# Kernel tuning notes

Measured on AMD Instinct MI355X. Metric: run time of the kernel, lower is better.

The kernel has to match this reference:

```python
import jax, jax.numpy as jnp
import numpy as np


def setup_inputs() -> dict:
    key = jax.random.key(0)
    ks = jax.random.split(key, 5)
    d_out, d_in = 4096, 4096
    r = min(d_out, d_in)
    B, T = 4, 2048
    x = jax.random.normal(ks[0], (B, T, d_in), dtype=jnp.float32)
    U = jax.random.normal(ks[1], (d_out, r), dtype=jnp.float32)
    S = jax.random.uniform(ks[2], (r,), dtype=jnp.float32)
    Vt = jax.random.normal(ks[3], (r, d_in), dtype=jnp.float32)
    epsilon = jnp.zeros((r,), dtype=jnp.float32)
    bias = jax.random.normal(ks[4], (d_out,), dtype=jnp.float32)
    return {"x": x, "U": U, "S": S, "Vt": Vt, "epsilon": epsilon, "bias": bias}


def reference(x, U, S, Vt, epsilon, bias):
    # w = U @ diag(S + epsilon) @ Vt  (diag folded as column scale of U)
    w = (U * (S + epsilon)[None, :]) @ Vt  # [d_out, d_in]
    # F.linear: y = x @ w.T + bias
    return jnp.einsum('btk,ok->bto', x, w) + bias
```

## Files before the change

kernel.cpp:

```cpp
#include <hip/hip_runtime.h>
#include <hip/hip_bf16.h>
#include <stdint.h>

typedef __attribute__((ext_vector_type(4))) float f32x4;
typedef __attribute__((ext_vector_type(8))) short short8v;

typedef __attribute__((address_space(1))) void gvoid;
typedef __attribute__((address_space(3))) void lvoid;

#define GLD16(gp, lp) __builtin_amdgcn_global_load_lds((const gvoid*)(gp), (lvoid*)(lp), 16, 0, 0)

__device__ __forceinline__ unsigned short f2bf(float f) {
    union { float ff; unsigned uu; } a; a.ff = f;
    unsigned u = a.uu;
    u += 0x7FFFu + ((u >> 16) & 1u);
    return (unsigned short)(u >> 16);
}

__global__ __launch_bounds__(256) void prep_u_kernel(
    const float* __restrict__ U, const float* __restrict__ S,
    const float* __restrict__ eps, unsigned short* __restrict__ Ub) {
    long idx = ((long)blockIdx.x * 256 + threadIdx.x) * 8;
    int r = (int)(idx & 4095);
    f32x4 u0 = *(const f32x4*)(U + idx);
    f32x4 u1 = *(const f32x4*)(U + idx + 4);
    f32x4 s0 = *(const f32x4*)(S + r);
    f32x4 s1 = *(const f32x4*)(S + r + 4);
    f32x4 e0 = *(const f32x4*)(eps + r);
    f32x4 e1 = *(const f32x4*)(eps + r + 4);
    union { uint4 v; unsigned short s[8]; } o;
#pragma unroll
    for (int j = 0; j < 4; ++j) {
        o.s[j]     = f2bf(u0[j] * (s0[j] + e0[j]));
        o.s[j + 4] = f2bf(u1[j] * (s1[j] + e1[j]));
    }
    *(uint4*)(Ub + idx) = o.v;
}

__global__ __launch_bounds__(256) void cvt_bf16_kernel(
    const float* __restrict__ src, unsigned short* __restrict__ dst) {
    long idx = ((long)blockIdx.x * 256 + threadIdx.x) * 8;
    f32x4 v0 = *(const f32x4*)(src + idx);
    f32x4 v1 = *(const f32x4*)(src + idx + 4);
    union { uint4 v; unsigned short s[8]; } o;
#pragma unroll
    for (int j = 0; j < 4; ++j) {
        o.s[j]     = f2bf(v0[j]);
        o.s[j + 4] = f2bf(v1[j]);
    }
    *(uint4*)(dst + idx) = o.v;
}

__global__ __launch_bounds__(256) void transpose_cvt_kernel(
    const float* __restrict__ src, unsigned short* __restrict__ dst) {
    __shared__ float tile[64][65];
    int tx = threadIdx.x & 63;
    int tq = threadIdx.x >> 6;
    int r0 = blockIdx.y << 6;
    int k0 = blockIdx.x << 6;
#pragma unroll
    for (int i = 0; i < 16; ++i) {
        int row = (i << 2) + tq;
        tile[row][tx] = src[(long)(r0 + row) * 4096 + k0 + tx];
    }
    __syncthreads();
#pragma unroll
    for (int i = 0; i < 16; ++i) {
        int krow = (i << 2) + tq;
        dst[(long)(k0 + krow) * 4096 + r0 + tx] = f2bf(tile[tx][krow]);
    }
}

#define MM(a, b, c) __builtin_amdgcn_mfma_f32_16x16x32_bf16(a, b, c, 0, 0, 0)

#define ACH(bf, kh) (As + ((bf) * 2 + (kh)) * 8192)
#define BCH(bf, kh) (Bs + ((bf) * 2 + (kh)) * 8192)

#define STAGE_A(bf, kh, koff) do { \
    const unsigned short* _s = A + gAr + (koff); \
    unsigned short* _d = ACH(bf, kh) + wave * 512; \
    GLD16(_s, _d); GLD16(_s + (long)128 * K, _d + 4096); } while (0)

#define STAGE_B(bf, kh, koff) do { \
    const unsigned short* _s = B + gBr + (koff); \
    unsigned short* _d = BCH(bf, kh) + wave * 512; \
    GLD16(_s, _d); GLD16(_s + (long)128 * K, _d + 4096); } while (0)

#define LOAD_A2(bf, ks) do { \
    const unsigned short* _p = ACH(bf, ks) + aBase; \
    _Pragma("unroll") \
    for (int _m = 0; _m < 4; ++_m) { \
        aR[0][_m] = *(const short8v*)(_p + _m * 512); \
        aR[1][_m] = *(const short8v*)(_p + _m * 512 + 2048); } } while (0)

#define READ_B(bf, ks) do { \
    const unsigned short* _p = BCH(bf, ks) + bBase; \
    _Pragma("unroll") \
    for (int _n = 0; _n < 4; ++_n) bR[_n] = *(const short8v*)(_p + _n * 512); } while (0)

#define PH_SYNC do { \
    __builtin_amdgcn_s_barrier(); \
    asm volatile("s_waitcnt lgkmcnt(0)" ::: "memory"); } while (0)

#define MFMA32 do { \
    __builtin_amdgcn_s_setprio(1); \
    _Pragma("unroll") \
    for (int _h = 0; _h < 2; ++_h) \
    _Pragma("unroll") \
    for (int _m = 0; _m < 4; ++_m) { \
        acc[_h * 4 + _m][0] = MM(aR[_h][_m], bR[0], acc[_h * 4 + _m][0]); \
        acc[_h * 4 + _m][1] = MM(aR[_h][_m], bR[1], acc[_h * 4 + _m][1]); \
        acc[_h * 4 + _m][2] = MM(aR[_h][_m], bR[2], acc[_h * 4 + _m][2]); \
        acc[_h * 4 + _m][3] = MM(aR[_h][_m], bR[3], acc[_h * 4 + _m][3]); \
    } \
    __builtin_amdgcn_s_setprio(0); } while (0)

#define VM4 asm volatile("s_waitcnt vmcnt(4)" ::: "memory")
#define PH_END __builtin_amdgcn_s_barrier()

template<int OUT_BF16, int BIAS>
__global__ __launch_bounds__(512, 2) void gemm256_kernel(
    const unsigned short* __restrict__ A,
    const unsigned short* __restrict__ B,
    void* __restrict__ Cv, const float* __restrict__ bias,
    int M, int N, int K) {
    __shared__ unsigned short As[4 * 8192];
    __shared__ unsigned short Bs[4 * 8192];

    const int tid  = threadIdx.x;
    const int wave = tid >> 6;
    const int lane = tid & 63;
    const int fr   = lane & 15;
    const int fq   = lane >> 4;

    const int nwg = gridDim.x;
    const int bid = blockIdx.x;
    const int cpx = nwg >> 3;
    const int wg  = (bid & 7) * cpx + (bid >> 3);
    const int ntn = N >> 8;
    const long m0 = (long)(wg / ntn) << 8;
    const long n0 = (long)(wg % ntn) << 8;

    const int wwr = wave >> 2;
    const int wwc = wave & 3;

    const int  rS  = tid >> 2;
    const int  sS  = (tid & 3) ^ ((rS >> 1) & 3);
    const long gAr = (m0 + rS) * K + sS * 8;
    const long gBr = (n0 + rS) * K + sS * 8;

    const int swz   = (fq ^ ((fr >> 1) & 3)) * 8;
    const int aBase = (wwr * 128 + fr) * 32 + swz;
    const int bBase = (wwc * 64 + fr) * 32 + swz;

    f32x4  acc[8][4] = {};
    short8v aR[2][4], bR[4];

    STAGE_A(0, 0, 0);  STAGE_B(0, 0, 0);
    STAGE_A(0, 1, 32); STAGE_B(0, 1, 32);
    STAGE_A(1, 0, 64); STAGE_B(1, 0, 64);
    VM4;
    __builtin_amdgcn_s_barrier();

    const int nIter = K >> 7;
    for (int i = 0; i < nIter; ++i) {
        const int kt1off = 128 * i + 96;
        int k3 = 128 * i + 128; if (k3 >= K) k3 -= K;
        int k5 = 128 * i + 160; if (k5 >= K) k5 -= K;
        int k7 = 128 * i + 192; if (k7 >= K) k7 -= K;

        LOAD_A2(0, 0); READ_B(0, 0); STAGE_A(1, 1, kt1off); STAGE_B(1, 1, kt1off);
        PH_SYNC; MFMA32; PH_END;
        LOAD_A2(0, 1); READ_B(0, 1); STAGE_A(0, 0, k3); STAGE_B(0, 0, k3);
        PH_SYNC; MFMA32; VM4; PH_END;
        LOAD_A2(1, 0); READ_B(1, 0); STAGE_A(0, 1, k5); STAGE_B(0, 1, k5);
        PH_SYNC; MFMA32; PH_END;
        LOAD_A2(1, 1); READ_B(1, 1); STAGE_A(1, 0, k7); STAGE_B(1, 0, k7);
        PH_SYNC; MFMA32; VM4; PH_END;
    }

#pragma unroll
    for (int nf = 0; nf < 4; ++nf) {
        const int col = (int)n0 + wwc * 64 + nf * 16 + fr;
        float bv = BIAS ? bias[col] : 0.0f;
#pragma unroll
        for (int mf = 0; mf < 8; ++mf) {
            f32x4 v = acc[mf][nf];
            long rowb = m0 + wwr * 128 + mf * 16 + fq * 4;
#pragma unroll
            for (int j = 0; j < 4; ++j) {
                float val = v[j] + bv;
                long off = (rowb + j) * N + col;
                if (OUT_BF16) ((unsigned short*)Cv)[off] = f2bf(val);
                else          ((float*)Cv)[off] = val;
            }
        }
    }
}

extern "C" void kernel_launch(void* const* d_in, const int* in_sizes, int n_in,
                              void* d_out, int out_size, void* d_ws, size_t ws_size,
                              hipStream_t stream) {
    const float* x    = (const float*)d_in[0];
    const float* U    = (const float*)d_in[1];
    const float* S    = (const float*)d_in[2];
    const float* Vt   = (const float*)d_in[3];
    const float* eps  = (const float*)d_in[4];
    const float* bias = (const float*)d_in[5];
    float* out = (float*)d_out;

    char* ws = (char*)d_ws;
    unsigned short* Ub  = (unsigned short*)(ws);
    unsigned short* VtT = (unsigned short*)(ws + (size_t)(32 << 20));
    unsigned short* Wb  = (unsigned short*)(ws + (size_t)(64 << 20));
    unsigned short* Xb  = (unsigned short*)(ws);

    prep_u_kernel<<<8192, 256, 0, stream>>>(U, S, eps, Ub);
    transpose_cvt_kernel<<<dim3(64, 64), 256, 0, stream>>>(Vt, VtT);
    gemm256_kernel<1, 0><<<256, 512, 0, stream>>>(Ub, VtT, (void*)Wb, nullptr,
                                                  4096, 4096, 4096);
    cvt_bf16_kernel<<<16384, 256, 0, stream>>>(x, Xb);
    gemm256_kernel<0, 1><<<512, 512, 0, stream>>>(Xb, Wb, (void*)out, bias,
                                                  8192, 4096, 4096);
}
```

Measured before the change: 469.2 us.

## Shrink GEMM tile to 256x128 with triple-buffered 32-K pipeline

Changes the GEMM block tile from 256x256 to 256x128. Each wave now covers 64x64 instead of 128x64, and the LDS staging becomes a 3-stage ring of 32-wide K chunks instead of 4 chunks in double pairs. Launch bounds move to 4 blocks per CU and the grid doubles, aiming for higher occupancy and more wave parallelism to hide memory latency. In exchange each block reuses less data per load and does more barrier phases per unit of work. The loop hardcodes K=4096 (42 groups of 96 plus a 2-step tail).

```diff
diff --git a/kernel.cpp b/kernel.cpp
--- a/kernel.cpp
+++ b/kernel.cpp
@@ -73,28 +73,26 @@
 
 #define MM(a, b, c) __builtin_amdgcn_mfma_f32_16x16x32_bf16(a, b, c, 0, 0, 0)
 
-#define ACH(bf, kh) (As + ((bf) * 2 + (kh)) * 8192)
-#define BCH(bf, kh) (Bs + ((bf) * 2 + (kh)) * 8192)
-
-#define STAGE_A(bf, kh, koff) do { \
+#define ACH(b) (As + (b) * 8192)
+#define BCH(b) (Bs + (b) * 4096)
+
+#define STAGE_A(b, koff) do { \
     const unsigned short* _s = A + gAr + (koff); \
-    unsigned short* _d = ACH(bf, kh) + wave * 512; \
+    unsigned short* _d = ACH(b) + wave * 512; \
     GLD16(_s, _d); GLD16(_s + (long)128 * K, _d + 4096); } while (0)
 
-#define STAGE_B(bf, kh, koff) do { \
+#define STAGE_B(b, koff) do { \
     const unsigned short* _s = B + gBr + (koff); \
-    unsigned short* _d = BCH(bf, kh) + wave * 512; \
-    GLD16(_s, _d); GLD16(_s + (long)128 * K, _d + 4096); } while (0)
-
-#define LOAD_A2(bf, ks) do { \
-    const unsigned short* _p = ACH(bf, ks) + aBase; \
+    unsigned short* _d = BCH(b) + wave * 512; \
+    GLD16(_s, _d); } while (0)
+
+#define LOAD_A(b) do { \
+    const unsigned short* _p = ACH(b) + aBase; \
     _Pragma("unroll") \
-    for (int _m = 0; _m < 4; ++_m) { \
-        aR[0][_m] = *(const short8v*)(_p + _m * 512); \
-        aR[1][_m] = *(const short8v*)(_p + _m * 512 + 2048); } } while (0)
-
-#define READ_B(bf, ks) do { \
-    const unsigned short* _p = BCH(bf, ks) + bBase; \
+    for (int _m = 0; _m < 4; ++_m) aR[_m] = *(const short8v*)(_p + _m * 512); } while (0)
+
+#define READ_B(b) do { \
+    const unsigned short* _p = BCH(b) + bBase; \
     _Pragma("unroll") \
     for (int _n = 0; _n < 4; ++_n) bR[_n] = *(const short8v*)(_p + _n * 512); } while (0)
 
@@ -102,30 +100,33 @@
     __builtin_amdgcn_s_barrier(); \
     asm volatile("s_waitcnt lgkmcnt(0)" ::: "memory"); } while (0)
 
-#define MFMA32 do { \
+#define MFMA16 do { \
     __builtin_amdgcn_s_setprio(1); \
     _Pragma("unroll") \
-    for (int _h = 0; _h < 2; ++_h) \
-    _Pragma("unroll") \
     for (int _m = 0; _m < 4; ++_m) { \
-        acc[_h * 4 + _m][0] = MM(aR[_h][_m], bR[0], acc[_h * 4 + _m][0]); \
-        acc[_h * 4 + _m][1] = MM(aR[_h][_m], bR[1], acc[_h * 4 + _m][1]); \
-        acc[_h * 4 + _m][2] = MM(aR[_h][_m], bR[2], acc[_h * 4 + _m][2]); \
-        acc[_h * 4 + _m][3] = MM(aR[_h][_m], bR[3], acc[_h * 4 + _m][3]); \
+        acc[_m][0] = MM(aR[_m], bR[0], acc[_m][0]); \
+        acc[_m][1] = MM(aR[_m], bR[1], acc[_m][1]); \
+        acc[_m][2] = MM(aR[_m], bR[2], acc[_m][2]); \
+        acc[_m][3] = MM(aR[_m], bR[3], acc[_m][3]); \
     } \
     __builtin_amdgcn_s_setprio(0); } while (0)
 
-#define VM4 asm volatile("s_waitcnt vmcnt(4)" ::: "memory")
+#define VM3 asm volatile("s_waitcnt vmcnt(3)" ::: "memory")
 #define PH_END __builtin_amdgcn_s_barrier()
 
+#define ITER(rb, sb, sk) do { \
+    LOAD_A(rb); READ_B(rb); \
+    STAGE_A(sb, sk); STAGE_B(sb, sk); \
+    PH_SYNC; MFMA16; VM3; PH_END; } while (0)
+
 template<int OUT_BF16, int BIAS>
-__global__ __launch_bounds__(512, 2) void gemm256_kernel(
+__global__ __launch_bounds__(512, 4) void gemm256_kernel(
     const unsigned short* __restrict__ A,
     const unsigned short* __restrict__ B,
     void* __restrict__ Cv, const float* __restrict__ bias,
     int M, int N, int K) {
-    __shared__ unsigned short As[4 * 8192];
-    __shared__ unsigned short Bs[4 * 8192];
+    __shared__ unsigned short As[3 * 8192];
+    __shared__ unsigned short Bs[3 * 4096];
 
     const int tid  = threadIdx.x;
     const int wave = tid >> 6;
@@ -137,12 +138,12 @@
     const int bid = blockIdx.x;
     const int cpx = nwg >> 3;
     const int wg  = (bid & 7) * cpx + (bid >> 3);
-    const int ntn = N >> 8;
+    const int ntn = N >> 7;
     const long m0 = (long)(wg / ntn) << 8;
-    const long n0 = (long)(wg % ntn) << 8;
-
-    const int wwr = wave >> 2;
-    const int wwc = wave & 3;
+    const long n0 = (long)(wg % ntn) << 7;
+
+    const int wwr = wave >> 1;
+    const int wwc = wave & 1;
 
     const int  rS  = tid >> 2;
     const int  sS  = (tid & 3) ^ ((rS >> 1) & 3);
@@ -150,43 +151,34 @@
     const long gBr = (n0 + rS) * K + sS * 8;
 
     const int swz   = (fq ^ ((fr >> 1) & 3)) * 8;
-    const int aBase = (wwr * 128 + fr) * 32 + swz;
+    const int aBase = (wwr * 64 + fr) * 32 + swz;
     const int bBase = (wwc * 64 + fr) * 32 + swz;
 
-    f32x4  acc[8][4] = {};
-    short8v aR[2][4], bR[4];
-
-    STAGE_A(0, 0, 0);  STAGE_B(0, 0, 0);
-    STAGE_A(0, 1, 32); STAGE_B(0, 1, 32);
-    STAGE_A(1, 0, 64); STAGE_B(1, 0, 64);
-    VM4;
+    f32x4  acc[4][4] = {};
+    short8v aR[4], bR[4];
+
+    STAGE_A(0, 0);  STAGE_B(0, 0);
+    STAGE_A(1, 32); STAGE_B(1, 32);
+    VM3;
     __builtin_amdgcn_s_barrier();
 
-    const int nIter = K >> 7;
-    for (int i = 0; i < nIter; ++i) {
-        const int kt1off = 128 * i + 96;
-        int k3 = 128 * i + 128; if (k3 >= K) k3 -= K;
-        int k5 = 128 * i + 160; if (k5 >= K) k5 -= K;
-        int k7 = 128 * i + 192; if (k7 >= K) k7 -= K;
-
-        LOAD_A2(0, 0); READ_B(0, 0); STAGE_A(1, 1, kt1off); STAGE_B(1, 1, kt1off);
-        PH_SYNC; MFMA32; PH_END;
-        LOAD_A2(0, 1); READ_B(0, 1); STAGE_A(0, 0, k3); STAGE_B(0, 0, k3);
-        PH_SYNC; MFMA32; VM4; PH_END;
-        LOAD_A2(1, 0); READ_B(1, 0); STAGE_A(0, 1, k5); STAGE_B(0, 1, k5);
-        PH_SYNC; MFMA32; PH_END;
-        LOAD_A2(1, 1); READ_B(1, 1); STAGE_A(1, 0, k7); STAGE_B(1, 0, k7);
-        PH_SYNC; MFMA32; VM4; PH_END;
-    }
+    for (int g = 0; g < 42; ++g) {
+        const int kb = 96 * g;
+        ITER(0, 2, kb + 64);
+        ITER(1, 0, kb + 96);
+        ITER(2, 1, kb + 128);
+    }
+    ITER(0, 2, 0);
+    ITER(1, 0, 0);
 
 #pragma unroll
     for (int nf = 0; nf < 4; ++nf) {
         const int col = (int)n0 + wwc * 64 + nf * 16 + fr;
         float bv = BIAS ? bias[col] : 0.0f;
 #pragma unroll
-        for (int mf = 0; mf < 8; ++mf) {
+        for (int mf = 0; mf < 4; ++mf) {
             f32x4 v = acc[mf][nf];
-            long rowb = m0 + wwr * 128 + mf * 16 + fq * 4;
+            long rowb = m0 + wwr * 64 + mf * 16 + fq * 4;
 #pragma unroll
             for (int j = 0; j < 4; ++j) {
                 float val = v[j] + bv;
@@ -217,9 +209,9 @@
 
     prep_u_kernel<<<8192, 256, 0, stream>>>(U, S, eps, Ub);
     transpose_cvt_kernel<<<dim3(64, 64), 256, 0, stream>>>(Vt, VtT);
-    gemm256_kernel<1, 0><<<256, 512, 0, stream>>>(Ub, VtT, (void*)Wb, nullptr,
+    gemm256_kernel<1, 0><<<512, 512, 0, stream>>>(Ub, VtT, (void*)Wb, nullptr,
                                                   4096, 4096, 4096);
     cvt_bf16_kernel<<<16384, 256, 0, stream>>>(x, Xb);
-    gemm256_kernel<0, 1><<<512, 512, 0, stream>>>(Xb, Wb, (void*)out, bias,
-                                                  8192, 4096, 4096);
-}
+    gemm256_kernel<0, 1><<<1024, 512, 0, stream>>>(Xb, Wb, (void*)out, bias,
+                                                   8192, 4096, 4096);
+}
```

Result: slower. 511.5 us (+9.0%).

## Double-buffer LDS fragment reads in registers to overlap ds_reads with MFMA

Applied to the files above, without the earlier changes.

The GEMM main loop is restructured so each phase issues the LDS reads for the next k-slice into a second register buffer while MFMAs consume the current one. Inline-asm ds_read_b128 with immediate offsets replaces the computed-address loads, and the per-phase barrier plus full lgkmcnt(0) wait becomes a partial lgkmcnt(12) wait with a sched_barrier. The LDS ring goes from a 2x2 buffer/half indexing to four flat slots. The aim is to hide LDS latency and remove one barrier per phase, at the cost of twice the fragment registers and a tighter ordering of the global-to-LDS staging against the reads.

```diff
diff --git a/kernel.cpp b/kernel.cpp
--- a/kernel.cpp
+++ b/kernel.cpp
@@ -73,50 +73,58 @@
 
 #define MM(a, b, c) __builtin_amdgcn_mfma_f32_16x16x32_bf16(a, b, c, 0, 0, 0)
 
-#define ACH(bf, kh) (As + ((bf) * 2 + (kh)) * 8192)
-#define BCH(bf, kh) (Bs + ((bf) * 2 + (kh)) * 8192)
-
-#define STAGE_A(bf, kh, koff) do { \
+#define ARG(r) (As + (r) * 8192)
+#define BRG(r) (Bs + (r) * 8192)
+
+#define STAGE_A(r, koff) do { \
     const unsigned short* _s = A + gAr + (koff); \
-    unsigned short* _d = ACH(bf, kh) + wave * 512; \
+    unsigned short* _d = ARG(r) + wave * 512; \
     GLD16(_s, _d); GLD16(_s + (long)128 * K, _d + 4096); } while (0)
 
-#define STAGE_B(bf, kh, koff) do { \
+#define STAGE_B(r, koff) do { \
     const unsigned short* _s = B + gBr + (koff); \
-    unsigned short* _d = BCH(bf, kh) + wave * 512; \
+    unsigned short* _d = BRG(r) + wave * 512; \
     GLD16(_s, _d); GLD16(_s + (long)128 * K, _d + 4096); } while (0)
 
-#define LOAD_A2(bf, ks) do { \
-    const unsigned short* _p = ACH(bf, ks) + aBase; \
-    _Pragma("unroll") \
-    for (int _m = 0; _m < 4; ++_m) { \
-        aR[0][_m] = *(const short8v*)(_p + _m * 512); \
-        aR[1][_m] = *(const short8v*)(_p + _m * 512 + 2048); } } while (0)
-
-#define READ_B(bf, ks) do { \
-    const unsigned short* _p = BCH(bf, ks) + bBase; \
-    _Pragma("unroll") \
-    for (int _n = 0; _n < 4; ++_n) bR[_n] = *(const short8v*)(_p + _n * 512); } while (0)
-
-#define PH_SYNC do { \
-    __builtin_amdgcn_s_barrier(); \
-    asm volatile("s_waitcnt lgkmcnt(0)" ::: "memory"); } while (0)
-
-#define MFMA32 do { \
+#define DSR(dst, base, imm) \
+    asm volatile("ds_read_b128 %0, %1 offset:%c2" \
+                 : "=v"(dst) : "v"(base), "i"(imm) : "memory")
+
+#define READ_AB(bk, R) do { \
+    DSR(aB[bk][0][0], aByte, (R)*16384 + 0);            \
+    DSR(aB[bk][0][1], aByte, (R)*16384 + 1024);         \
+    DSR(aB[bk][0][2], aByte, (R)*16384 + 2048);         \
+    DSR(aB[bk][0][3], aByte, (R)*16384 + 3072);         \
+    DSR(aB[bk][1][0], aByte, (R)*16384 + 4096);         \
+    DSR(aB[bk][1][1], aByte, (R)*16384 + 5120);         \
+    DSR(aB[bk][1][2], aByte, (R)*16384 + 6144);         \
+    DSR(aB[bk][1][3], aByte, (R)*16384 + 7168);         \
+    DSR(bB[bk][0],    bByte, (R)*16384 + 0);            \
+    DSR(bB[bk][1],    bByte, (R)*16384 + 1024);         \
+    DSR(bB[bk][2],    bByte, (R)*16384 + 2048);         \
+    DSR(bB[bk][3],    bByte, (R)*16384 + 3072); } while (0)
+
+#define MFMA32(bk) do { \
     __builtin_amdgcn_s_setprio(1); \
     _Pragma("unroll") \
     for (int _h = 0; _h < 2; ++_h) \
     _Pragma("unroll") \
     for (int _m = 0; _m < 4; ++_m) { \
-        acc[_h * 4 + _m][0] = MM(aR[_h][_m], bR[0], acc[_h * 4 + _m][0]); \
-        acc[_h * 4 + _m][1] = MM(aR[_h][_m], bR[1], acc[_h * 4 + _m][1]); \
-        acc[_h * 4 + _m][2] = MM(aR[_h][_m], bR[2], acc[_h * 4 + _m][2]); \
-        acc[_h * 4 + _m][3] = MM(aR[_h][_m], bR[3], acc[_h * 4 + _m][3]); \
+        acc[_h*4+_m][0] = MM(aB[bk][_h][_m], bB[bk][0], acc[_h*4+_m][0]); \
+        acc[_h*4+_m][1] = MM(aB[bk][_h][_m], bB[bk][1], acc[_h*4+_m][1]); \
+        acc[_h*4+_m][2] = MM(aB[bk][_h][_m], bB[bk][2], acc[_h*4+_m][2]); \
+        acc[_h*4+_m][3] = MM(aB[bk][_h][_m], bB[bk][3], acc[_h*4+_m][3]); \
     } \
     __builtin_amdgcn_s_setprio(0); } while (0)
 
-#define VM4 asm volatile("s_waitcnt vmcnt(4)" ::: "memory")
-#define PH_END __builtin_amdgcn_s_barrier()
+#define PHASE(rN, sb, rS, sk, cb) do { \
+    STAGE_A(rS, sk); STAGE_B(rS, sk); \
+    READ_AB(sb, rN); \
+    asm volatile("s_waitcnt lgkmcnt(12)" ::: "memory"); \
+    __builtin_amdgcn_sched_barrier(0); \
+    MFMA32(cb); \
+    asm volatile("s_waitcnt vmcnt(4)" ::: "memory"); \
+    __builtin_amdgcn_s_barrier(); } while (0)
 
 template<int OUT_BF16, int BIAS>
 __global__ __launch_bounds__(512, 2) void gemm256_kernel(
@@ -152,31 +160,30 @@
     const int swz   = (fq ^ ((fr >> 1) & 3)) * 8;
     const int aBase = (wwr * 128 + fr) * 32 + swz;
     const int bBase = (wwc * 64 + fr) * 32 + swz;
+    const unsigned aByte = (unsigned)(uintptr_t)(As + aBase);
+    const unsigned bByte = (unsigned)(uintptr_t)(Bs + bBase);
 
     f32x4  acc[8][4] = {};
-    short8v aR[2][4], bR[4];
-
-    STAGE_A(0, 0, 0);  STAGE_B(0, 0, 0);
-    STAGE_A(0, 1, 32); STAGE_B(0, 1, 32);
-    STAGE_A(1, 0, 64); STAGE_B(1, 0, 64);
-    VM4;
+    short8v aB[2][2][4], bB[2][4];
+
+    STAGE_A(0, 0);  STAGE_B(0, 0);
+    STAGE_A(1, 32); STAGE_B(1, 32);
+    STAGE_A(2, 64); STAGE_B(2, 64);
+    asm volatile("s_waitcnt vmcnt(4)" ::: "memory");
     __builtin_amdgcn_s_barrier();
+    READ_AB(0, 0);
 
     const int nIter = K >> 7;
     for (int i = 0; i < nIter; ++i) {
-        const int kt1off = 128 * i + 96;
-        int k3 = 128 * i + 128; if (k3 >= K) k3 -= K;
-        int k5 = 128 * i + 160; if (k5 >= K) k5 -= K;
-        int k7 = 128 * i + 192; if (k7 >= K) k7 -= K;
-
-        LOAD_A2(0, 0); READ_B(0, 0); STAGE_A(1, 1, kt1off); STAGE_B(1, 1, kt1off);
-        PH_SYNC; MFMA32; PH_END;
-        LOAD_A2(0, 1); READ_B(0, 1); STAGE_A(0, 0, k3); STAGE_B(0, 0, k3);
-        PH_SYNC; MFMA32; VM4; PH_END;
-        LOAD_A2(1, 0); READ_B(1, 0); STAGE_A(0, 1, k5); STAGE_B(0, 1, k5);
-        PH_SYNC; MFMA32; PH_END;
-        LOAD_A2(1, 1); READ_B(1, 1); STAGE_A(1, 0, k7); STAGE_B(1, 0, k7);
-        PH_SYNC; MFMA32; VM4; PH_END;
+        const int kA = 128 * i + 96;
+        int k0n = 128 * i + 128; if (k0n >= K) k0n -= K;
+        int k1n = 128 * i + 160; if (k1n >= K) k1n -= K;
+        int k2n = 128 * i + 192; if (k2n >= K) k2n -= K;
+
+        PHASE(1, 1, 3, kA,  0);
+        PHASE(2, 0, 0, k0n, 1);
+        PHASE(3, 1, 1, k1n, 0);
+        PHASE(0, 0, 2, k2n, 1);
     }
 
 #pragma unroll
```

New measurement: 442.1 us. -5.8%, faster.
